# Optimization experiments

Hardware: AMD Instinct MI355X
Metric: run time of the kernel (lower is better)

## Reference

```python
import jax, jax.numpy as jnp
import numpy as np
import math

D_MODEL = 1024
N_HEADS = 16
D_HEAD = D_MODEL // N_HEADS
WINDOW_LEN = 128
DILATION = 4
SEQ = 3072
BATCH = 1


def setup_inputs() -> dict:
    key = jax.random.key(0)
    ks = jax.random.split(key, 10)
    def xavier(k, shape):
        fan_out, fan_in = shape
        lim = math.sqrt(6.0 / (fan_in + fan_out))
        return jax.random.uniform(k, shape, jnp.float32, -lim, lim)
    return {
        "x": jax.random.normal(ks[0], (SEQ, BATCH, D_MODEL), jnp.float32),
        "beta": 0.1 * jax.random.normal(ks[1], (N_HEADS,), jnp.float32),
        "Wq": xavier(ks[2], (D_MODEL, D_MODEL)),
        "bq": jnp.zeros((D_MODEL,), jnp.float32),
        "Wk": xavier(ks[3], (D_MODEL, D_MODEL)),
        "bk": jnp.zeros((D_MODEL,), jnp.float32),
        "Wv": xavier(ks[4], (D_MODEL, D_MODEL)),
        "bv": jnp.zeros((D_MODEL,), jnp.float32),
        "Wo": xavier(ks[5], (D_MODEL, D_MODEL)),
        "bo": jnp.zeros((D_MODEL,), jnp.float32),
    }


def _causal_windowed_bias(seq_len):
    # allowed iff 0 <= (i-j), (i-j)//dilation < window_len, (i-j) % dilation == 0
    idx = jnp.arange(seq_len)
    diff = idx[:, None] - idx[None, :]
    allowed = (diff >= 0) & (diff // DILATION < WINDOW_LEN) & (diff % DILATION == 0)
    return jnp.where(allowed, 0.0, -jnp.inf).astype(jnp.float32)  # [S, S]


def reference(x, beta, Wq, bq, Wk, bk, Wv, bv, Wo, bo):
    s, b, d = x.shape
    # projections: nn.Linear => x @ W.T + b
    def split_heads(t):  # [s, b, h*dh] -> [b, h, s, dh]
        return t.reshape(s, b, N_HEADS, D_HEAD).transpose(1, 2, 0, 3)
    q = split_heads(x @ Wq.T + bq)
    k = split_heads(x @ Wk.T + bk)
    v = split_heads(x @ Wv.T + bv)
    # beta scaling folded into q, attention uses scale=1.0
    q = q / (math.sqrt(D_HEAD) * jnp.exp(beta)[None, :, None, None])
    bias = _causal_windowed_bias(s)  # [S, S]
    scores = jnp.einsum('bhsd,bhtd->bhst', q, k) + bias
    attn = jax.nn.softmax(scores, axis=-1)
    ctx = jnp.einsum('bhst,bhtd->bhsd', attn, v)  # [b, h, s, dh]
    ctx = ctx.transpose(2, 0, 1, 3).reshape(s, b, d)  # [s, b, d_model]
    return ctx @ Wo.T + bo
```

## Files before the change

kernel.cpp:

```cpp
#include <hip/hip_runtime.h>
#include <math.h>

#define SEQ   3072
#define DM    1024
#define NH    16
#define DH    64
#define WIN   128
#define DIL   4
#define TSUB  768

typedef __attribute__((ext_vector_type(8))) short    short8;
typedef __attribute__((ext_vector_type(8))) _Float16 half8;
typedef __attribute__((ext_vector_type(4))) _Float16 half4;
typedef __attribute__((ext_vector_type(4))) float    floatx4;

__device__ __forceinline__ float bf2f(unsigned short u) {
    return __uint_as_float(((unsigned)u) << 16);
}
__device__ __forceinline__ unsigned short f2bf(float f) {
    unsigned u = __float_as_uint(f);
    return (unsigned short)((u + 0x7FFFu + ((u >> 16) & 1u)) >> 16);
}
__device__ __forceinline__ unsigned short f2h(float f) {
    _Float16 h = (_Float16)f;
    return __builtin_bit_cast(unsigned short, h);
}

__device__ __forceinline__ void gload_lds16(const void* g, void* l) {
    __builtin_amdgcn_global_load_lds(
        (const __attribute__((address_space(1))) void*)g,
        (__attribute__((address_space(3))) void*)l, 16, 0, 0);
}

__global__ __launch_bounds__(256) void convert_kernel(
    const float* __restrict__ x,  const float* __restrict__ Wq,
    const float* __restrict__ Wk, const float* __restrict__ Wv,
    const float* __restrict__ Wo,
    ushort* __restrict__ xb,  ushort* __restrict__ Wqb,
    ushort* __restrict__ Wkb, ushort* __restrict__ Wvb,
    ushort* __restrict__ Wob)
{
    const int NX = SEQ * DM / 4;
    const int NW = DM * DM / 4;
    const int NT = NX + 4 * NW;
    for (int i = blockIdx.x * 256 + threadIdx.x; i < NT; i += gridDim.x * 256) {
        const float* s; ushort* d; int o;
        if (i < NX)               { s = x;  d = xb;  o = i; }
        else if (i < NX + NW)     { s = Wq; d = Wqb; o = i - NX; }
        else if (i < NX + 2 * NW) { s = Wk; d = Wkb; o = i - NX - 2 * NW + NW; }
        else if (i < NX + 3 * NW) { s = Wv; d = Wvb; o = i - NX - 2 * NW; }
        else                      { s = Wo; d = Wob; o = i - NX - 3 * NW; }
        float4 v = ((const float4*)s)[o];
        ushort4 u = { f2bf(v.x), f2bf(v.y), f2bf(v.z), f2bf(v.w) };
        ((ushort4*)d)[o] = u;
    }
}

struct QkvSmem {
    ushort As[2][128][64];
    ushort Bs[2][64][64];
};

template<bool QSCALE, bool F16OUT>
__device__ __forceinline__ void gemm_qkv_body(QkvSmem& sm,
                                              const ushort* __restrict__ A,
                                              const ushort* __restrict__ W,
                                              const float* __restrict__ bias,
                                              const float* __restrict__ beta,
                                              ushort* __restrict__ C,
                                              int bx, int by)
{
    const int tid  = threadIdx.x;
    const int lane = tid & 63, w = tid >> 6;
    const int ln15 = lane & 15, quad = lane >> 4;
    const int wm = w >> 1, wn = w & 1;

    const int rl = lane >> 3, cl = lane & 7;
    const ushort* aRow[4];
#pragma unroll
    for (int i = 0; i < 4; ++i) {
        int row   = w * 32 + 8 * i + rl;
        int chunk = cl ^ ((row >> 1) & 7);
        aRow[i] = A + (size_t)(by * 128 + row) * DM + chunk * 8;
    }
    const ushort* bRow[2];
#pragma unroll
    for (int i = 0; i < 2; ++i) {
        int row   = w * 16 + 8 * i + rl;
        int chunk = cl ^ ((row >> 1) & 7);
        bRow[i] = W + (size_t)(bx * 64 + row) * DM + chunk * 8;
    }

    const int col0 = bx * 64 + wn * 32 + ln15;
    float eb0 = bias[col0];
    float eb1 = bias[col0 + 16];
    float escale = QSCALE ? 0.125f * __expf(-beta[bx]) : 1.0f;
    asm volatile("" : "+v"(eb0), "+v"(eb1), "+v"(escale));

    const floatx4 zero = {0.f, 0.f, 0.f, 0.f};
    floatx4 acc[4][2];
#pragma unroll
    for (int i = 0; i < 4; ++i)
#pragma unroll
        for (int j = 0; j < 2; ++j) acc[i][j] = zero;

#pragma unroll
    for (int i = 0; i < 4; ++i) gload_lds16(aRow[i], &sm.As[0][w * 32 + 8 * i][0]);
#pragma unroll
    for (int i = 0; i < 2; ++i) gload_lds16(bRow[i], &sm.Bs[0][w * 16 + 8 * i][0]);

    const int rf = (ln15 >> 1) & 7;
#pragma unroll 2
    for (int t = 0; t < 16; ++t) {
        const int cur = t & 1, nxt = cur ^ 1;
        if (t < 15) {
            const int ko = (t + 1) * 64;
#pragma unroll
            for (int i = 0; i < 4; ++i) gload_lds16(aRow[i] + ko, &sm.As[nxt][w * 32 + 8 * i][0]);
#pragma unroll
            for (int i = 0; i < 2; ++i) gload_lds16(bRow[i] + ko, &sm.Bs[nxt][w * 16 + 8 * i][0]);
            __builtin_amdgcn_sched_barrier(0);
            asm volatile("s_waitcnt vmcnt(6)" ::: "memory");
        } else {
            __builtin_amdgcn_sched_barrier(0);
            asm volatile("s_waitcnt vmcnt(0)" ::: "memory");
        }
        __builtin_amdgcn_sched_barrier(0);
        __builtin_amdgcn_s_barrier();
#pragma unroll
        for (int s = 0; s < 2; ++s) {
            short8 af[4], bf[2];
#pragma unroll
            for (int i = 0; i < 4; ++i)
                af[i] = *(const short8*)&sm.As[cur][wm * 64 + i * 16 + ln15][((s * 4 + quad) ^ rf) * 8];
#pragma unroll
            for (int j = 0; j < 2; ++j)
                bf[j] = *(const short8*)&sm.Bs[cur][wn * 32 + j * 16 + ln15][((s * 4 + quad) ^ rf) * 8];
#pragma unroll
            for (int i = 0; i < 4; ++i)
#pragma unroll
                for (int j = 0; j < 2; ++j)
                    acc[i][j] = __builtin_amdgcn_mfma_f32_16x16x32_bf16(af[i], bf[j], acc[i][j], 0, 0, 0);
        }
        asm volatile("s_waitcnt lgkmcnt(0)" ::: "memory");
        __builtin_amdgcn_sched_barrier(0);
        __builtin_amdgcn_s_barrier();
    }

#pragma unroll
    for (int j = 0; j < 2; ++j) {
        const int col = col0 + j * 16;
        const float b = j ? eb1 : eb0;
#pragma unroll
        for (int i = 0; i < 4; ++i) {
            const int row0 = by * 128 + wm * 64 + i * 16 + quad * 4;
#pragma unroll
            for (int rg = 0; rg < 4; ++rg) {
                float vv = (acc[i][j][rg] + b) * escale;
                C[(size_t)(row0 + rg) * DM + col] = F16OUT ? f2h(vv) : f2bf(vv);
            }
        }
    }
}

__global__ __launch_bounds__(256, 3) void qkv_kernel(
    const ushort* __restrict__ xb,
    const ushort* __restrict__ Wqb, const float* __restrict__ bq,
    const ushort* __restrict__ Wkb, const float* __restrict__ bk,
    const ushort* __restrict__ Wvb, const float* __restrict__ bv,
    const float* __restrict__ beta,
    ushort* __restrict__ q, ushort* __restrict__ k, ushort* __restrict__ v)
{
    __shared__ QkvSmem sm;
    const int lid = blockIdx.x;
    const int xcd = lid & 7, s = lid >> 3;
    const int G   = xcd * 9 + (s >> 4);
    const int by  = G % 24, z = G / 24;
    const int bx  = s & 15;
    const ushort* W = (z == 0) ? Wqb : (z == 1) ? Wkb : Wvb;
    const float*  b = (z == 0) ? bq  : (z == 1) ? bk  : bv;
    ushort*       C = (z == 0) ? q   : (z == 1) ? k   : v;
    if (z == 0)
        gemm_qkv_body<true , false>(sm, xb, W, b, beta, C, bx, by);
    else if (z == 1)
        gemm_qkv_body<false, false>(sm, xb, W, b, nullptr, C, bx, by);
    else
        gemm_qkv_body<false, true >(sm, xb, W, b, nullptr, C, bx, by);
}

__global__ __launch_bounds__(256, 3) void out_kernel(
    const ushort* __restrict__ ctxb, const ushort* __restrict__ Wob,
    const float* __restrict__ bo, float* __restrict__ out)
{
    __shared__ ushort As[2][64][64];
    __shared__ ushort Bs[2][64][64];

    const int tid  = threadIdx.x;
    const int lane = tid & 63, w = tid >> 6;
    const int ln15 = lane & 15, quad = lane >> 4;
    const int wm = w >> 1, wn = w & 1;

    const int lid = blockIdx.x;
    const int xcd = lid & 7, s0 = lid >> 3;
    const int by  = xcd * 6 + (s0 >> 4);
    const int bx  = s0 & 15;

    const int rl = lane >> 3, cl = lane & 7;
    const ushort* aRow[2]; const ushort* bRow[2];
#pragma unroll
    for (int i = 0; i < 2; ++i) {
        int row   = w * 16 + 8 * i + rl;
        int chunk = cl ^ ((row >> 1) & 7);
        aRow[i] = ctxb + (size_t)(by * 64 + row) * DM + chunk * 8;
        bRow[i] = Wob  + (size_t)(bx * 64 + row) * DM + chunk * 8;
    }

    const int col0 = bx * 64 + wn * 32 + ln15;
    float eb0 = bo[col0];
    float eb1 = bo[col0 + 16];
    asm volatile("" : "+v"(eb0), "+v"(eb1));

    const floatx4 zero = {0.f, 0.f, 0.f, 0.f};
    floatx4 acc[2][2];
#pragma unroll
    for (int i = 0; i < 2; ++i)
#pragma unroll
        for (int j = 0; j < 2; ++j) acc[i][j] = zero;

#pragma unroll
    for (int i = 0; i < 2; ++i) {
        gload_lds16(aRow[i], &As[0][w * 16 + 8 * i][0]);
        gload_lds16(bRow[i], &Bs[0][w * 16 + 8 * i][0]);
    }

    const int rf = (ln15 >> 1) & 7;
#pragma unroll 2
    for (int t = 0; t < 16; ++t) {
        const int cur = t & 1, nxt = cur ^ 1;
        if (t < 15) {
            const int ko = (t + 1) * 64;
#pragma unroll
            for (int i = 0; i < 2; ++i) {
                gload_lds16(aRow[i] + ko, &As[nxt][w * 16 + 8 * i][0]);
                gload_lds16(bRow[i] + ko, &Bs[nxt][w * 16 + 8 * i][0]);
            }
            __builtin_amdgcn_sched_barrier(0);
            asm volatile("s_waitcnt vmcnt(4)" ::: "memory");
        } else {
            __builtin_amdgcn_sched_barrier(0);
            asm volatile("s_waitcnt vmcnt(0)" ::: "memory");
        }
        __builtin_amdgcn_sched_barrier(0);
        __builtin_amdgcn_s_barrier();
#pragma unroll
        for (int s = 0; s < 2; ++s) {
            short8 af[2], bf[2];
#pragma unroll
            for (int i = 0; i < 2; ++i)
                af[i] = *(const short8*)&As[cur][wm * 32 + i * 16 + ln15][((s * 4 + quad) ^ rf) * 8];
#pragma unroll
            for (int j = 0; j < 2; ++j)
                bf[j] = *(const short8*)&Bs[cur][wn * 32 + j * 16 + ln15][((s * 4 + quad) ^ rf) * 8];
#pragma unroll
            for (int i = 0; i < 2; ++i)
#pragma unroll
                for (int j = 0; j < 2; ++j)
                    acc[i][j] = __builtin_amdgcn_mfma_f32_16x16x32_bf16(af[i], bf[j], acc[i][j], 0, 0, 0);
        }
        asm volatile("s_waitcnt lgkmcnt(0)" ::: "memory");
        __builtin_amdgcn_sched_barrier(0);
        __builtin_amdgcn_s_barrier();
    }

#pragma unroll
    for (int j = 0; j < 2; ++j) {
        const int col = col0 + j * 16;
        const float b = j ? eb1 : eb0;
#pragma unroll
        for (int i = 0; i < 2; ++i) {
            const int row0 = by * 64 + wm * 32 + i * 16 + quad * 4;
#pragma unroll
            for (int rg = 0; rg < 4; ++rg)
                out[(size_t)(row0 + rg) * DM + col] = acc[i][j][rg] + b;
        }
    }
}

struct AttnSmem {
    union {
        ushort Ks[160 * 64];
        ushort Vs[40 * 256];
    } u;
    float  S[32][163];
    ushort P[32][168];
    float  Rsum[32];
};

__global__ __launch_bounds__(256, 3) void attn_kernel(
    const ushort* __restrict__ q, const ushort* __restrict__ k,
    const ushort* __restrict__ v, ushort* __restrict__ ctx)
{
    __shared__ AttnSmem sm;

    const int tid  = threadIdx.x;
    const int lane = tid & 63, w = tid >> 6;
    const int ln15 = lane & 15, quad = lane >> 4;

    const int lid = blockIdx.x;
    const int xcd = lid & 7, s0 = lid >> 3;
    const int h   = xcd * 2 + (s0 / 96);
    const int rem = s0 % 96;
    const int t0  = (rem % 24) * 32;
    const int r   = rem / 24;
    const int hoff = h * DH;

    {
        const int kr = lane >> 3;
        const int swz = ((lane & 7) ^ kr) * 8;
#pragma unroll
        for (int ci = w * 5; ci < w * 5 + 5; ++ci) {
            int key = ci * 8 + kr;
            long grow = 4L * (t0 - 128 + key) + r;
            gload_lds16(k + grow * DM + hoff + swz, &sm.u.Ks[ci * 512]);
        }
    }

    const int qt = w >> 1;
    short8 qf0, qf1;
    {
        int qrow = qt * 16 + ln15;
        const ushort* gq = q + (4L * (t0 + qrow) + r) * DM + hoff + quad * 8;
        qf0 = *(const short8*)gq;
        qf1 = *(const short8*)(gq + 32);
    }

    __syncthreads();

    {
        const floatx4 zero = {0.f, 0.f, 0.f, 0.f};
        const int kt0 = (w & 1) * 5;
        const int lb  = ln15 & 7;
#pragma unroll
        for (int kk2 = 0; kk2 < 5; ++kk2) {
            const int kt  = kt0 + kk2;
            const int key = kt * 16 + ln15;
            short8 b0 = *(const short8*)&sm.u.Ks[key * 64 + ((quad ^ lb) << 3)];
            short8 b1 = *(const short8*)&sm.u.Ks[key * 64 + (((4 + quad) ^ lb) << 3)];
            floatx4 acc = zero;
            acc = __builtin_amdgcn_mfma_f32_16x16x32_bf16(qf0, b0, acc, 0, 0, 0);
            acc = __builtin_amdgcn_mfma_f32_16x16x32_bf16(qf1, b1, acc, 0, 0, 0);
            const int tp = t0 - 128 + key;
#pragma unroll
            for (int rg = 0; rg < 4; ++rg) {
                int qrow = qt * 16 + quad * 4 + rg;
                int tq = t0 + qrow;
                bool ok = (tp >= 0) && (tp <= tq) && (tp > tq - WIN);
                sm.S[qrow][key] = ok ? acc[rg] : -1e30f;
            }
        }
    }

    __syncthreads();

    {
#pragma unroll
        for (int i = 0; i < 5; ++i) {
            const int o  = w * 5 + i;
            const int c  = o * 64 + lane;
            const int hh = c & 1, jj = (c >> 1) & 3, qq = (c >> 3) & 3;
            const int T  = c >> 5;
            const int p  = T & 1, dtt = (T >> 1) & 3, kc = T >> 3;
            const int key = kc * 32 + qq * 8 + p * 4 + jj;
            const int dim = dtt * 16 + hh * 8;
            long grow = 4L * (t0 - 128 + key) + r;
            gload_lds16(v + grow * DM + hoff + dim, &sm.u.Vs[o * 512]);
        }
    }

    {
        const int sq = tid >> 3, part = tid & 7;
        float sreg[20];
        float m = -1e30f;
#pragma unroll
        for (int j = 0; j < 20; ++j) {
            sreg[j] = sm.S[sq][part + 8 * j];
            m = fmaxf(m, sreg[j]);
        }
#pragma unroll
        for (int o = 1; o < 8; o <<= 1) m = fmaxf(m, __shfl_xor(m, o));
        float sum = 0.f;
#pragma unroll
        for (int j = 0; j < 20; ++j) {
            float e = __expf(sreg[j] - m);
            sm.P[sq][part + 8 * j] = f2h(e);
            sum += e;
        }
#pragma unroll
        for (int o = 1; o < 8; o <<= 1) sum += __shfl_xor(sum, o);
        if (part == 0) sm.Rsum[sq] = 1.0f / sum;
    }

    __syncthreads();

    {
        const floatx4 zero = {0.f, 0.f, 0.f, 0.f};
        const int qtp = w & 1, dh = w >> 1;
        floatx4 o0 = zero, o1 = zero;
        const unsigned vbase =
            (unsigned)(size_t)(__attribute__((address_space(3))) ushort*)&sm.u.Vs[0]
            + lane * 8 + dh * 2048;
#pragma unroll
        for (int kc = 0; kc < 5; ++kc) {
            half8 pa = *(const half8*)&sm.P[qtp * 16 + ln15][kc * 32 + quad * 8];
            half4 a0, a1, b0, b1;
            asm volatile(
                "ds_read_b64_tr_b16 %0, %4\n\t"
                "ds_read_b64_tr_b16 %1, %4 offset:512\n\t"
                "ds_read_b64_tr_b16 %2, %4 offset:1024\n\t"
                "ds_read_b64_tr_b16 %3, %4 offset:1536\n\t"
                "s_waitcnt lgkmcnt(0)"
                : "=&v"(a0), "=&v"(a1), "=&v"(b0), "=&v"(b1)
                : "v"(vbase + kc * 4096));
            __builtin_amdgcn_sched_barrier(0);
            half8 vb0 = __builtin_shufflevector(a0, a1, 0, 1, 2, 3, 4, 5, 6, 7);
            half8 vb1 = __builtin_shufflevector(b0, b1, 0, 1, 2, 3, 4, 5, 6, 7);
            o0 = __builtin_amdgcn_mfma_f32_16x16x32_f16(pa, vb0, o0, 0, 0, 0);
            o1 = __builtin_amdgcn_mfma_f32_16x16x32_f16(pa, vb1, o1, 0, 0, 0);
        }
#pragma unroll
        for (int rg = 0; rg < 4; ++rg) {
            int qrow = qtp * 16 + quad * 4 + rg;
            float rs = sm.Rsum[qrow];
            long orow = 4L * (t0 + qrow) + r;
            ushort* cp = ctx + orow * DM + hoff + dh * 32 + ln15;
            cp[0]  = f2bf(o0[rg] * rs);
            cp[16] = f2bf(o1[rg] * rs);
        }
    }
}

extern "C" void kernel_launch(void* const* d_in, const int* in_sizes, int n_in,
                              void* d_out, int out_size, void* d_ws, size_t ws_size,
                              hipStream_t stream)
{
    const float* x    = (const float*)d_in[0];
    const float* beta = (const float*)d_in[1];
    const float* Wq   = (const float*)d_in[2];
    const float* bq   = (const float*)d_in[3];
    const float* Wk   = (const float*)d_in[4];
    const float* bk   = (const float*)d_in[5];
    const float* Wv   = (const float*)d_in[6];
    const float* bv   = (const float*)d_in[7];
    const float* Wo   = (const float*)d_in[8];
    const float* bo   = (const float*)d_in[9];

    ushort* qb   = (ushort*)d_ws;
    ushort* kb   = qb   + (size_t)SEQ * DM;
    ushort* vb   = kb   + (size_t)SEQ * DM;
    ushort* ctxb = vb   + (size_t)SEQ * DM;
    ushort* xb   = ctxb + (size_t)SEQ * DM;
    ushort* Wqb  = xb   + (size_t)SEQ * DM;
    ushort* Wkb  = Wqb  + (size_t)DM * DM;
    ushort* Wvb  = Wkb  + (size_t)DM * DM;
    ushort* Wob  = Wvb  + (size_t)DM * DM;
    float*  out  = (float*)d_out;

    convert_kernel<<<dim3(2048), 256, 0, stream>>>(x, Wq, Wk, Wv, Wo, xb, Wqb, Wkb, Wvb, Wob);

    qkv_kernel<<<dim3(1152), 256, 0, stream>>>(xb, Wqb, bq, Wkb, bk, Wvb, bv, beta, qb, kb, vb);

    attn_kernel<<<dim3(1536), 256, 0, stream>>>(qb, kb, vb, ctxb);

    out_kernel<<<dim3(768), 256, 0, stream>>>(ctxb, Wob, bo, out);
}
```

Before: 139.8 us.

## Compute softmax in registers and overlap V load with QK in attention

The attention kernel no longer writes the masked score matrix to shared memory. Each wave now runs softmax on its half of the keys in registers using cross-lane shuffles. The two halves are merged with per-row max and sum rescale factors that are applied to P in fp16 before the PV MFMA. K and V move into separate shared buffers instead of a union, so the V load can be issued before the QK compute, with explicit vmcnt waits and raw barriers. The cost is more shared memory per block, which may reduce occupancy, and slightly different fp16 rounding.

Result: no change. 139.8 us (median of 2 runs) (+0.0%).

```diff
diff --git a/kernel.cpp b/kernel.cpp
--- a/kernel.cpp
+++ b/kernel.cpp
@@ -287,13 +287,12 @@
 }
 
 struct AttnSmem {
-    union {
-        ushort Ks[160 * 64];
-        ushort Vs[40 * 256];
-    } u;
-    float  S[32][163];
+    ushort Ks[160 * 64];
+    ushort Vs[40 * 256];
     ushort P[32][168];
-    float  Rsum[32];
+    float  mh[2][32];
+    float  sh[2][32];
+    float  f0[32], f1[32], rsum[32];
 };
 
 __global__ __launch_bounds__(256, 3) void attn_kernel(
@@ -321,9 +320,10 @@
         for (int ci = w * 5; ci < w * 5 + 5; ++ci) {
             int key = ci * 8 + kr;
             long grow = 4L * (t0 - 128 + key) + r;
-            gload_lds16(k + grow * DM + hoff + swz, &sm.u.Ks[ci * 512]);
-        }
-    }
+            gload_lds16(k + grow * DM + hoff + swz, &sm.Ks[ci * 512]);
+        }
+    }
+    __builtin_amdgcn_sched_barrier(0);
 
     const int qt = w >> 1;
     short8 qf0, qf1;
@@ -333,34 +333,7 @@
         qf0 = *(const short8*)gq;
         qf1 = *(const short8*)(gq + 32);
     }
-
-    __syncthreads();
-
-    {
-        const floatx4 zero = {0.f, 0.f, 0.f, 0.f};
-        const int kt0 = (w & 1) * 5;
-        const int lb  = ln15 & 7;
-#pragma unroll
-        for (int kk2 = 0; kk2 < 5; ++kk2) {
-            const int kt  = kt0 + kk2;
-            const int key = kt * 16 + ln15;
-            short8 b0 = *(const short8*)&sm.u.Ks[key * 64 + ((quad ^ lb) << 3)];
-            short8 b1 = *(const short8*)&sm.u.Ks[key * 64 + (((4 + quad) ^ lb) << 3)];
-            floatx4 acc = zero;
-            acc = __builtin_amdgcn_mfma_f32_16x16x32_bf16(qf0, b0, acc, 0, 0, 0);
-            acc = __builtin_amdgcn_mfma_f32_16x16x32_bf16(qf1, b1, acc, 0, 0, 0);
-            const int tp = t0 - 128 + key;
-#pragma unroll
-            for (int rg = 0; rg < 4; ++rg) {
-                int qrow = qt * 16 + quad * 4 + rg;
-                int tq = t0 + qrow;
-                bool ok = (tp >= 0) && (tp <= tq) && (tp > tq - WIN);
-                sm.S[qrow][key] = ok ? acc[rg] : -1e30f;
-            }
-        }
-    }
-
-    __syncthreads();
+    __builtin_amdgcn_sched_barrier(0);
 
     {
 #pragma unroll
@@ -373,45 +346,100 @@
             const int key = kc * 32 + qq * 8 + p * 4 + jj;
             const int dim = dtt * 16 + hh * 8;
             long grow = 4L * (t0 - 128 + key) + r;
-            gload_lds16(v + grow * DM + hoff + dim, &sm.u.Vs[o * 512]);
-        }
-    }
+            gload_lds16(v + grow * DM + hoff + dim, &sm.Vs[o * 512]);
+        }
+    }
+    __builtin_amdgcn_sched_barrier(0);
+
+    asm volatile("s_waitcnt vmcnt(5)" ::: "memory");
+    __builtin_amdgcn_sched_barrier(0);
+    __builtin_amdgcn_s_barrier();
 
     {
-        const int sq = tid >> 3, part = tid & 7;
-        float sreg[20];
-        float m = -1e30f;
-#pragma unroll
-        for (int j = 0; j < 20; ++j) {
-            sreg[j] = sm.S[sq][part + 8 * j];
-            m = fmaxf(m, sreg[j]);
-        }
-#pragma unroll
-        for (int o = 1; o < 8; o <<= 1) m = fmaxf(m, __shfl_xor(m, o));
-        float sum = 0.f;
-#pragma unroll
-        for (int j = 0; j < 20; ++j) {
-            float e = __expf(sreg[j] - m);
-            sm.P[sq][part + 8 * j] = f2h(e);
-            sum += e;
-        }
-#pragma unroll
-        for (int o = 1; o < 8; o <<= 1) sum += __shfl_xor(sum, o);
-        if (part == 0) sm.Rsum[sq] = 1.0f / sum;
-    }
-
-    __syncthreads();
+        const floatx4 zero = {0.f, 0.f, 0.f, 0.f};
+        const int kt0 = (w & 1) * 5;
+        const int lb  = ln15 & 7;
+        float sv[5][4];
+#pragma unroll
+        for (int kk2 = 0; kk2 < 5; ++kk2) {
+            const int kt  = kt0 + kk2;
+            const int key = kt * 16 + ln15;
+            short8 b0 = *(const short8*)&sm.Ks[key * 64 + ((quad ^ lb) << 3)];
+            short8 b1 = *(const short8*)&sm.Ks[key * 64 + (((4 + quad) ^ lb) << 3)];
+            floatx4 acc = zero;
+            acc = __builtin_amdgcn_mfma_f32_16x16x32_bf16(qf0, b0, acc, 0, 0, 0);
+            acc = __builtin_amdgcn_mfma_f32_16x16x32_bf16(qf1, b1, acc, 0, 0, 0);
+            const int tp = t0 - 128 + key;
+#pragma unroll
+            for (int rg = 0; rg < 4; ++rg) {
+                int tq = t0 + qt * 16 + quad * 4 + rg;
+                bool ok = (tp >= 0) && (tp <= tq) && (tp > tq - WIN);
+                sv[kk2][rg] = ok ? acc[rg] : -1e30f;
+            }
+        }
+        float mh4[4], sh4[4];
+#pragma unroll
+        for (int rg = 0; rg < 4; ++rg) {
+            float m = sv[0][rg];
+#pragma unroll
+            for (int kk2 = 1; kk2 < 5; ++kk2) m = fmaxf(m, sv[kk2][rg]);
+#pragma unroll
+            for (int o = 1; o < 16; o <<= 1) m = fmaxf(m, __shfl_xor(m, o));
+            float s = 0.f;
+            const int qrow = qt * 16 + quad * 4 + rg;
+#pragma unroll
+            for (int kk2 = 0; kk2 < 5; ++kk2) {
+                float e = __expf(sv[kk2][rg] - m);
+                s += e;
+                sm.P[qrow][(kt0 + kk2) * 16 + ln15] = f2h(e);
+            }
+#pragma unroll
+            for (int o = 1; o < 16; o <<= 1) s += __shfl_xor(s, o);
+            mh4[rg] = m; sh4[rg] = s;
+        }
+        if (ln15 == 0) {
+#pragma unroll
+            for (int rg = 0; rg < 4; ++rg) {
+                const int qrow = qt * 16 + quad * 4 + rg;
+                sm.mh[w & 1][qrow] = mh4[rg];
+                sm.sh[w & 1][qrow] = sh4[rg];
+            }
+        }
+    }
+
+    asm volatile("s_waitcnt lgkmcnt(0)" ::: "memory");
+    __builtin_amdgcn_sched_barrier(0);
+    __builtin_amdgcn_s_barrier();
+
+    if (tid < 32) {
+        float m0 = sm.mh[0][tid], m1 = sm.mh[1][tid];
+        float s0 = sm.sh[0][tid], s1 = sm.sh[1][tid];
+        float m  = fmaxf(m0, m1);
+        float g0 = __expf(m0 - m), g1 = __expf(m1 - m);
+        sm.f0[tid] = g0;
+        sm.f1[tid] = g1;
+        sm.rsum[tid] = 1.0f / (s0 * g0 + s1 * g1);
+    }
+
+    asm volatile("s_waitcnt vmcnt(0) lgkmcnt(0)" ::: "memory");
+    __builtin_amdgcn_sched_barrier(0);
+    __builtin_amdgcn_s_barrier();
 
     {
         const floatx4 zero = {0.f, 0.f, 0.f, 0.f};
         const int qtp = w & 1, dh = w >> 1;
+        const int prow = qtp * 16 + ln15;
+        const float vf0 = sm.f0[prow], vf1 = sm.f1[prow];
         floatx4 o0 = zero, o1 = zero;
         const unsigned vbase =
-            (unsigned)(size_t)(__attribute__((address_space(3))) ushort*)&sm.u.Vs[0]
+            (unsigned)(size_t)(__attribute__((address_space(3))) ushort*)&sm.Vs[0]
             + lane * 8 + dh * 2048;
 #pragma unroll
         for (int kc = 0; kc < 5; ++kc) {
-            half8 pa = *(const half8*)&sm.P[qtp * 16 + ln15][kc * 32 + quad * 8];
+            half8 pa = *(const half8*)&sm.P[prow][kc * 32 + quad * 8];
+            float ff = (kc < 2) ? vf0 : (kc > 2) ? vf1 : (quad < 2 ? vf0 : vf1);
+            _Float16 fh = (_Float16)ff;
+            pa *= fh;
             half4 a0, a1, b0, b1;
             asm volatile(
                 "ds_read_b64_tr_b16 %0, %4\n\t"
@@ -430,7 +458,7 @@
 #pragma unroll
         for (int rg = 0; rg < 4; ++rg) {
             int qrow = qtp * 16 + quad * 4 + rg;
-            float rs = sm.Rsum[qrow];
+            float rs = sm.rsum[qrow];
             long orow = 4L * (t0 + qrow) + r;
             ushort* cp = ctx + orow * DM + hoff + dh * 32 + ln15;
             cp[0]  = f2bf(o0[rg] * rs);
```
